# Kernel optimization log

Hardware: AMD Instinct MI355X
Metric: run time of the kernel (lower is better)

Reference implementation:

```python
import jax, jax.numpy as jnp
import numpy as np


def setup_inputs() -> dict:
    key = jax.random.key(0)
    k1, k2, k3 = jax.random.split(key, 3)
    B, H, L, OUT = 4096, 2048, 8, 1024
    x = jax.random.normal(k1, (B, H), dtype=jnp.float32)
    W = jax.random.normal(k2, (L, H, H), dtype=jnp.float32)
    beta = jax.random.normal(k3, (H, OUT), dtype=jnp.float32)
    return {"x": x, "W": W, "beta": beta}


def _fcn_forward(x, W, beta):
    h = W.shape[-1]
    scale = 1.0 / jnp.sqrt(jnp.asarray(h, x.dtype))
    # Linear1d: (x[:,None]*W).sum(-1)/sqrt(h) == x @ W.T / sqrt(h); then ReLU.
    def layer(y, Wi):
        y = jax.nn.relu(jnp.einsum('bi,oi->bo', y, Wi) * scale)
        return y, None
    y, _ = jax.lax.scan(layer, x, W)
    # readout: y @ beta / h
    return jnp.einsum('bh,ho->bo', y, beta) / h


def reference(x, W, beta):
    return _fcn_forward(x, W, beta)
```

## Files before the change

kernel.cpp:

```cpp
#include <hip/hip_runtime.h>
#include <cstdint>
#include <cstddef>

typedef __bf16          bf16x8  __attribute__((ext_vector_type(8)));
typedef float           f32x4   __attribute__((ext_vector_type(4)));
typedef unsigned short  u16x8   __attribute__((ext_vector_type(8)));

__device__ __forceinline__ unsigned short f32_bf16_rne(float f) {
  union { float f; unsigned u; } v; v.f = f;
  unsigned u = v.u + 0x7FFFu + ((v.u >> 16) & 1u);
  return (unsigned short)(u >> 16);
}

__global__ void cvt_f32_bf16(const float* __restrict__ in,
                             unsigned short* __restrict__ out, int n8) {
  int idx = blockIdx.x * 256 + threadIdx.x;
  int stride = gridDim.x * 256;
  for (int i = idx; i < n8; i += stride) {
    float4 a = ((const float4*)in)[2 * (size_t)i];
    float4 b = ((const float4*)in)[2 * (size_t)i + 1];
    u16x8 o;
    o[0] = f32_bf16_rne(a.x); o[1] = f32_bf16_rne(a.y);
    o[2] = f32_bf16_rne(a.z); o[3] = f32_bf16_rne(a.w);
    o[4] = f32_bf16_rne(b.x); o[5] = f32_bf16_rne(b.y);
    o[6] = f32_bf16_rne(b.z); o[7] = f32_bf16_rne(b.w);
    *(u16x8*)(out + (size_t)i * 8) = o;
  }
}

__global__ void cvt_transpose(const float* __restrict__ in,
                              unsigned short* __restrict__ out, int H, int O) {
  __shared__ float tile[32][33];
  int o0 = blockIdx.x * 32, h0 = blockIdx.y * 32;
  int tx = threadIdx.x & 31, ty = threadIdx.x >> 5;
  #pragma unroll
  for (int i = ty; i < 32; i += 8)
    tile[i][tx] = in[(size_t)(h0 + i) * O + (o0 + tx)];
  __syncthreads();
  #pragma unroll
  for (int i = ty; i < 32; i += 8)
    out[(size_t)(o0 + i) * H + (h0 + tx)] = f32_bf16_rne(tile[tx][i]);
}


#define GLOAD(gp, lp)                                                   \
  __builtin_amdgcn_global_load_lds(                                     \
      (const __attribute__((address_space(1))) void*)(gp),              \
      (__attribute__((address_space(3))) void*)(lp), 16, 0, 0)

#define MFMA16 __builtin_amdgcn_mfma_f32_16x16x32_bf16

#define PHASE(MH, STAGE)                                                      \
  do {                                                                        \
    bf16x8 a00 = *(const bf16x8*)(cA + aBase + ((MH)*2+0)*1024 + c0);         \
    bf16x8 a01 = *(const bf16x8*)(cA + aBase + ((MH)*2+0)*1024 + c1);         \
    bf16x8 a10 = *(const bf16x8*)(cA + aBase + ((MH)*2+1)*1024 + c0);         \
    bf16x8 a11 = *(const bf16x8*)(cA + aBase + ((MH)*2+1)*1024 + c1);         \
    bf16x8 b00 = *(const bf16x8*)(cB + bBase + 0*1024 + c0);                  \
    bf16x8 b01 = *(const bf16x8*)(cB + bBase + 0*1024 + c1);                  \
    bf16x8 b10 = *(const bf16x8*)(cB + bBase + 1*1024 + c0);                  \
    bf16x8 b11 = *(const bf16x8*)(cB + bBase + 1*1024 + c1);                  \
    bf16x8 b20 = *(const bf16x8*)(cB + bBase + 2*1024 + c0);                  \
    bf16x8 b21 = *(const bf16x8*)(cB + bBase + 2*1024 + c1);                  \
    bf16x8 b30 = *(const bf16x8*)(cB + bBase + 3*1024 + c0);                  \
    bf16x8 b31 = *(const bf16x8*)(cB + bBase + 3*1024 + c1);                  \
    STAGE                                                                     \
    __builtin_amdgcn_sched_barrier(0);                                        \
    __builtin_amdgcn_s_barrier();                                             \
    asm volatile("s_waitcnt lgkmcnt(0)" ::: "memory");                        \
    __builtin_amdgcn_sched_barrier(0);                                        \
    __builtin_amdgcn_s_setprio(1);                                            \
    acc[(MH)*2+0][0] = MFMA16(a00, b00, acc[(MH)*2+0][0], 0, 0, 0);           \
    acc[(MH)*2+0][1] = MFMA16(a00, b10, acc[(MH)*2+0][1], 0, 0, 0);           \
    acc[(MH)*2+0][2] = MFMA16(a00, b20, acc[(MH)*2+0][2], 0, 0, 0);           \
    acc[(MH)*2+0][3] = MFMA16(a00, b30, acc[(MH)*2+0][3], 0, 0, 0);           \
    acc[(MH)*2+1][0] = MFMA16(a10, b00, acc[(MH)*2+1][0], 0, 0, 0);           \
    acc[(MH)*2+1][1] = MFMA16(a10, b10, acc[(MH)*2+1][1], 0, 0, 0);           \
    acc[(MH)*2+1][2] = MFMA16(a10, b20, acc[(MH)*2+1][2], 0, 0, 0);           \
    acc[(MH)*2+1][3] = MFMA16(a10, b30, acc[(MH)*2+1][3], 0, 0, 0);           \
    acc[(MH)*2+0][0] = MFMA16(a01, b01, acc[(MH)*2+0][0], 0, 0, 0);           \
    acc[(MH)*2+0][1] = MFMA16(a01, b11, acc[(MH)*2+0][1], 0, 0, 0);           \
    acc[(MH)*2+0][2] = MFMA16(a01, b21, acc[(MH)*2+0][2], 0, 0, 0);           \
    acc[(MH)*2+0][3] = MFMA16(a01, b31, acc[(MH)*2+0][3], 0, 0, 0);           \
    acc[(MH)*2+1][0] = MFMA16(a11, b01, acc[(MH)*2+1][0], 0, 0, 0);           \
    acc[(MH)*2+1][1] = MFMA16(a11, b11, acc[(MH)*2+1][1], 0, 0, 0);           \
    acc[(MH)*2+1][2] = MFMA16(a11, b21, acc[(MH)*2+1][2], 0, 0, 0);           \
    acc[(MH)*2+1][3] = MFMA16(a11, b31, acc[(MH)*2+1][3], 0, 0, 0);           \
    __builtin_amdgcn_s_setprio(0);                                            \
    __builtin_amdgcn_sched_barrier(0);                                        \
    __builtin_amdgcn_s_barrier();                                             \
  } while (0)

__global__ __launch_bounds__(512, 2)
void gemm256x128(const unsigned short* __restrict__ A,
                 const unsigned short* __restrict__ B,
                 unsigned short* __restrict__ Cp, int N, int K, float scale) {
  __shared__ __bf16 As[3 * 256 * 64] __attribute__((aligned(16)));
  __shared__ __bf16 Bs[3 * 128 * 64] __attribute__((aligned(16)));

  const int tid  = threadIdx.x;
  const int lane = tid & 63;
  const int wave = tid >> 6;
  const int wr   = wave >> 1;
  const int wc   = wave & 1;
  const int l16  = lane & 15;
  const int kgrp = lane >> 4;

  const int p   = blockIdx.y * gridDim.x + blockIdx.x;
  const int lin = (p & 7) * (256 >> 3) + (p >> 3);
  const int brow0 = (lin >> 4) * 256;
  const int bcol0 = (lin & 15) * 128;

  const int xorv  = (l16 & 7) << 3;
  const int c0    = (kgrp * 8) ^ xorv;
  const int c1    = (32 + kgrp * 8) ^ xorv;
  const int aBase = (wr * 64 + l16) * 64;
  const int bBase = (wc * 64 + l16) * 64;

  const int srow = tid >> 3;
  const int scol = ((tid & 7) * 8) ^ ((srow & 7) << 3);
  const unsigned short* gA0 = A + (size_t)(brow0 +   0 + srow) * K + scol;
  const unsigned short* gA1 = A + (size_t)(brow0 +  64 + srow) * K + scol;
  const unsigned short* gA2 = A + (size_t)(brow0 + 128 + srow) * K + scol;
  const unsigned short* gA3 = A + (size_t)(brow0 + 192 + srow) * K + scol;
  const unsigned short* gB0 = B + (size_t)(bcol0 +   0 + srow) * K + scol;
  const unsigned short* gB1 = B + (size_t)(bcol0 +  64 + srow) * K + scol;

  f32x4 acc[4][4] = {};

  const int NT = K >> 6;

  {
    GLOAD(gA0, &As[0 * 4096 + tid * 8]);
    GLOAD(gA1, &As[1 * 4096 + tid * 8]);
    GLOAD(gA2, &As[2 * 4096 + tid * 8]);
    GLOAD(gA3, &As[3 * 4096 + tid * 8]);
    GLOAD(gB0, &Bs[0 * 4096 + tid * 8]);
    GLOAD(gB1, &Bs[1 * 4096 + tid * 8]);
    GLOAD(gA0 + 64, &As[16384 + 0 * 4096 + tid * 8]);
    GLOAD(gA1 + 64, &As[16384 + 1 * 4096 + tid * 8]);
    GLOAD(gA2 + 64, &As[16384 + 2 * 4096 + tid * 8]);
    GLOAD(gA3 + 64, &As[16384 + 3 * 4096 + tid * 8]);
    GLOAD(gB0 + 64, &Bs[8192 + 0 * 4096 + tid * 8]);
    GLOAD(gB1 + 64, &Bs[8192 + 1 * 4096 + tid * 8]);
    asm volatile("s_waitcnt vmcnt(6)" ::: "memory");
    __builtin_amdgcn_s_barrier();
  }

  int s = 0;
  for (int t = 0; t < NT; ++t) {
    const __bf16* cA = &As[s * 16384];
    const __bf16* cB = &Bs[s * 8192];
    int su = s + 2; if (su >= 3) su -= 3;
    __bf16* dA = &As[su * 16384];
    __bf16* dB = &Bs[su * 8192];
    const bool stg = (t < NT - 2);
    const size_t ko = (size_t)(t + 2) * 64;

    PHASE(0,
      if (stg) {
        GLOAD(gA0 + ko, dA + 0 * 4096 + tid * 8);
        GLOAD(gA1 + ko, dA + 1 * 4096 + tid * 8);
        GLOAD(gA2 + ko, dA + 2 * 4096 + tid * 8);
      }
    );
    PHASE(1,
      if (stg) {
        GLOAD(gA3 + ko, dA + 3 * 4096 + tid * 8);
        GLOAD(gB0 + ko, dB + 0 * 4096 + tid * 8);
        GLOAD(gB1 + ko, dB + 1 * 4096 + tid * 8);
        asm volatile("s_waitcnt vmcnt(6)" ::: "memory");
      } else if (t == NT - 2) {
        asm volatile("s_waitcnt vmcnt(0)" ::: "memory");
      }
    );
    s = s + 1; if (s == 3) s = 0;
  }

  const int crow0 = brow0 + wr * 64 + kgrp * 4;
  const int ccol0 = bcol0 + wc * 64 + l16;
  #pragma unroll
  for (int m = 0; m < 4; ++m)
    #pragma unroll
    for (int n = 0; n < 4; ++n)
      #pragma unroll
      for (int j = 0; j < 4; ++j) {
        float v = acc[m][n][j] * scale;
        v = v > 0.0f ? v : 0.0f;
        Cp[(size_t)(crow0 + m * 16 + j) * N + (ccol0 + n * 16)] = f32_bf16_rne(v);
      }
}

__global__ __launch_bounds__(256)
void gemm_bt_f32(const unsigned short* __restrict__ A,
                 const unsigned short* __restrict__ B,
                 float* __restrict__ C, int N, int K, float scale) {
  __shared__ __bf16 As[128 * 32] __attribute__((aligned(16)));
  __shared__ __bf16 Bs[128 * 32] __attribute__((aligned(16)));

  const int tid  = threadIdx.x;
  const int lane = tid & 63;
  const int wave = tid >> 6;
  const int wr   = wave >> 1, wc = wave & 1;
  const int l16  = lane & 15, kgrp = lane >> 4;

  const int brow0 = blockIdx.y * 128;
  const int bcol0 = blockIdx.x * 128;

  const int offb  = wave * 2048 + lane * 16;
  const int srow  = offb >> 6;
  const int selem = (offb & 63) >> 1;
  const unsigned short* gA0 = A + (size_t)(brow0 + srow) * K + selem;
  const unsigned short* gA1 = A + (size_t)(brow0 + srow + 16) * K + selem;
  const unsigned short* gB0 = B + (size_t)(bcol0 + srow) * K + selem;
  const unsigned short* gB1 = B + (size_t)(bcol0 + srow + 16) * K + selem;
  __bf16* lA0 = &As[wave * 1024];
  __bf16* lA1 = &As[wave * 1024 + 512];
  __bf16* lB0 = &Bs[wave * 1024];
  __bf16* lB1 = &Bs[wave * 1024 + 512];

  f32x4 acc[4][4] = {};
  const int aoff = (wr * 64 + l16) * 32 + kgrp * 8;
  const int boff = (wc * 64 + l16) * 32 + kgrp * 8;

  for (int k0 = 0; k0 < K; k0 += 32) {
    GLOAD(gA0 + k0, lA0);
    GLOAD(gA1 + k0, lA1);
    GLOAD(gB0 + k0, lB0);
    GLOAD(gB1 + k0, lB1);
    asm volatile("s_waitcnt vmcnt(0)" ::: "memory");
    __syncthreads();

    bf16x8 af[4], bfv[4];
    #pragma unroll
    for (int m = 0; m < 4; ++m)
      af[m] = *(const bf16x8*)(As + aoff + m * 16 * 32);
    #pragma unroll
    for (int n = 0; n < 4; ++n)
      bfv[n] = *(const bf16x8*)(Bs + boff + n * 16 * 32);
    #pragma unroll
    for (int m = 0; m < 4; ++m)
      #pragma unroll
      for (int n = 0; n < 4; ++n)
        acc[m][n] = MFMA16(af[m], bfv[n], acc[m][n], 0, 0, 0);
    __syncthreads();
  }

  const int crow0 = brow0 + wr * 64 + kgrp * 4;
  const int ccol0 = bcol0 + wc * 64 + l16;
  #pragma unroll
  for (int m = 0; m < 4; ++m)
    #pragma unroll
    for (int n = 0; n < 4; ++n)
      #pragma unroll
      for (int j = 0; j < 4; ++j)
        C[(size_t)(crow0 + m * 16 + j) * N + (ccol0 + n * 16)] =
            acc[m][n][j] * scale;
}

extern "C" void kernel_launch(void* const* d_in, const int* in_sizes, int n_in,
                              void* d_out, int out_size, void* d_ws, size_t ws_size,
                              hipStream_t stream) {
  const float* x    = (const float*)d_in[0];
  const float* W    = (const float*)d_in[1];
  const float* beta = (const float*)d_in[2];
  float* out = (float*)d_out;

  const int Bn = 4096, H = 2048, L = 8, O = 1024;

  unsigned short* y0    = (unsigned short*)d_ws;
  unsigned short* y1    = y0 + (size_t)Bn * H;
  unsigned short* Wb    = y1 + (size_t)Bn * H;
  unsigned short* betaT = Wb + (size_t)H * H;

  {
    int n8 = Bn * H / 8;
    int grid = (n8 + 255) / 256;
    if (grid > 2048) grid = 2048;
    cvt_f32_bf16<<<grid, 256, 0, stream>>>(x, y0, n8);
  }
  cvt_transpose<<<dim3(O / 32, H / 32), 256, 0, stream>>>(beta, betaT, H, O);

  const float s1 = 0.02209708691207961f;
  unsigned short* yin = y0;
  unsigned short* yout = y1;
  for (int l = 0; l < L; ++l) {
    int n8 = H * H / 8;
    int grid = (n8 + 255) / 256;
    if (grid > 2048) grid = 2048;
    cvt_f32_bf16<<<grid, 256, 0, stream>>>(W + (size_t)l * H * H, Wb, n8);
    gemm256x128<<<dim3(H / 128, Bn / 256), 512, 0, stream>>>(yin, Wb, yout, H, H, s1);
    unsigned short* t = yin; yin = yout; yout = t;
  }
  gemm_bt_f32<<<dim3(O / 128, Bn / 128), 256, 0, stream>>>(yin, betaT, out, O, H,
                                                           1.0f / 2048.0f);
}
```

Measured before the change: 428.9 us.

## Transpose GEMM block tile to 128x256 and split phases along K

```diff
diff --git a/kernel.cpp b/kernel.cpp
--- a/kernel.cpp
+++ b/kernel.cpp
@@ -42,7 +42,6 @@
     out[(size_t)(o0 + i) * H + (h0 + tx)] = f32_bf16_rne(tile[tx][i]);
 }
 
-
 #define GLOAD(gp, lp)                                                   \
   __builtin_amdgcn_global_load_lds(                                     \
       (const __attribute__((address_space(1))) void*)(gp),              \
@@ -50,70 +49,66 @@
 
 #define MFMA16 __builtin_amdgcn_mfma_f32_16x16x32_bf16
 
-#define PHASE(MH, STAGE)                                                      \
+
+#define PHASE(KK, STAGE)                                                      \
   do {                                                                        \
-    bf16x8 a00 = *(const bf16x8*)(cA + aBase + ((MH)*2+0)*1024 + c0);         \
-    bf16x8 a01 = *(const bf16x8*)(cA + aBase + ((MH)*2+0)*1024 + c1);         \
-    bf16x8 a10 = *(const bf16x8*)(cA + aBase + ((MH)*2+1)*1024 + c0);         \
-    bf16x8 a11 = *(const bf16x8*)(cA + aBase + ((MH)*2+1)*1024 + c1);         \
-    bf16x8 b00 = *(const bf16x8*)(cB + bBase + 0*1024 + c0);                  \
-    bf16x8 b01 = *(const bf16x8*)(cB + bBase + 0*1024 + c1);                  \
-    bf16x8 b10 = *(const bf16x8*)(cB + bBase + 1*1024 + c0);                  \
-    bf16x8 b11 = *(const bf16x8*)(cB + bBase + 1*1024 + c1);                  \
-    bf16x8 b20 = *(const bf16x8*)(cB + bBase + 2*1024 + c0);                  \
-    bf16x8 b21 = *(const bf16x8*)(cB + bBase + 2*1024 + c1);                  \
-    bf16x8 b30 = *(const bf16x8*)(cB + bBase + 3*1024 + c0);                  \
-    bf16x8 b31 = *(const bf16x8*)(cB + bBase + 3*1024 + c1);                  \
+    const int c = cc##KK;                                                     \
+    bf16x8 a0 = *(const bf16x8*)(cA + aBase + 0 * 1024 + c);                  \
+    bf16x8 a1 = *(const bf16x8*)(cA + aBase + 1 * 1024 + c);                  \
+    bf16x8 a2 = *(const bf16x8*)(cA + aBase + 2 * 1024 + c);                  \
+    bf16x8 a3 = *(const bf16x8*)(cA + aBase + 3 * 1024 + c);                  \
+    bf16x8 b0 = *(const bf16x8*)(cB + bBase + 0 * 1024 + c);                  \
+    bf16x8 b1 = *(const bf16x8*)(cB + bBase + 1 * 1024 + c);                  \
+    bf16x8 b2 = *(const bf16x8*)(cB + bBase + 2 * 1024 + c);                  \
+    bf16x8 b3 = *(const bf16x8*)(cB + bBase + 3 * 1024 + c);                  \
     STAGE                                                                     \
     __builtin_amdgcn_sched_barrier(0);                                        \
     __builtin_amdgcn_s_barrier();                                             \
     asm volatile("s_waitcnt lgkmcnt(0)" ::: "memory");                        \
     __builtin_amdgcn_sched_barrier(0);                                        \
     __builtin_amdgcn_s_setprio(1);                                            \
-    acc[(MH)*2+0][0] = MFMA16(a00, b00, acc[(MH)*2+0][0], 0, 0, 0);           \
-    acc[(MH)*2+0][1] = MFMA16(a00, b10, acc[(MH)*2+0][1], 0, 0, 0);           \
-    acc[(MH)*2+0][2] = MFMA16(a00, b20, acc[(MH)*2+0][2], 0, 0, 0);           \
-    acc[(MH)*2+0][3] = MFMA16(a00, b30, acc[(MH)*2+0][3], 0, 0, 0);           \
-    acc[(MH)*2+1][0] = MFMA16(a10, b00, acc[(MH)*2+1][0], 0, 0, 0);           \
-    acc[(MH)*2+1][1] = MFMA16(a10, b10, acc[(MH)*2+1][1], 0, 0, 0);           \
-    acc[(MH)*2+1][2] = MFMA16(a10, b20, acc[(MH)*2+1][2], 0, 0, 0);           \
-    acc[(MH)*2+1][3] = MFMA16(a10, b30, acc[(MH)*2+1][3], 0, 0, 0);           \
-    acc[(MH)*2+0][0] = MFMA16(a01, b01, acc[(MH)*2+0][0], 0, 0, 0);           \
-    acc[(MH)*2+0][1] = MFMA16(a01, b11, acc[(MH)*2+0][1], 0, 0, 0);           \
-    acc[(MH)*2+0][2] = MFMA16(a01, b21, acc[(MH)*2+0][2], 0, 0, 0);           \
-    acc[(MH)*2+0][3] = MFMA16(a01, b31, acc[(MH)*2+0][3], 0, 0, 0);           \
-    acc[(MH)*2+1][0] = MFMA16(a11, b01, acc[(MH)*2+1][0], 0, 0, 0);           \
-    acc[(MH)*2+1][1] = MFMA16(a11, b11, acc[(MH)*2+1][1], 0, 0, 0);           \
-    acc[(MH)*2+1][2] = MFMA16(a11, b21, acc[(MH)*2+1][2], 0, 0, 0);           \
-    acc[(MH)*2+1][3] = MFMA16(a11, b31, acc[(MH)*2+1][3], 0, 0, 0);           \
+    acc[0][0] = MFMA16(a0, b0, acc[0][0], 0, 0, 0);                           \
+    acc[0][1] = MFMA16(a0, b1, acc[0][1], 0, 0, 0);                           \
+    acc[0][2] = MFMA16(a0, b2, acc[0][2], 0, 0, 0);                           \
+    acc[0][3] = MFMA16(a0, b3, acc[0][3], 0, 0, 0);                           \
+    acc[1][0] = MFMA16(a1, b0, acc[1][0], 0, 0, 0);                           \
+    acc[1][1] = MFMA16(a1, b1, acc[1][1], 0, 0, 0);                           \
+    acc[1][2] = MFMA16(a1, b2, acc[1][2], 0, 0, 0);                           \
+    acc[1][3] = MFMA16(a1, b3, acc[1][3], 0, 0, 0);                           \
+    acc[2][0] = MFMA16(a2, b0, acc[2][0], 0, 0, 0);                           \
+    acc[2][1] = MFMA16(a2, b1, acc[2][1], 0, 0, 0);                           \
+    acc[2][2] = MFMA16(a2, b2, acc[2][2], 0, 0, 0);                           \
+    acc[2][3] = MFMA16(a2, b3, acc[2][3], 0, 0, 0);                           \
+    acc[3][0] = MFMA16(a3, b0, acc[3][0], 0, 0, 0);                           \
+    acc[3][1] = MFMA16(a3, b1, acc[3][1], 0, 0, 0);                           \
+    acc[3][2] = MFMA16(a3, b2, acc[3][2], 0, 0, 0);                           \
+    acc[3][3] = MFMA16(a3, b3, acc[3][3], 0, 0, 0);                           \
     __builtin_amdgcn_s_setprio(0);                                            \
     __builtin_amdgcn_sched_barrier(0);                                        \
     __builtin_amdgcn_s_barrier();                                             \
   } while (0)
 
 __global__ __launch_bounds__(512, 2)
-void gemm256x128(const unsigned short* __restrict__ A,
+void gemm128x256(const unsigned short* __restrict__ A,
                  const unsigned short* __restrict__ B,
                  unsigned short* __restrict__ Cp, int N, int K, float scale) {
-  __shared__ __bf16 As[3 * 256 * 64] __attribute__((aligned(16)));
-  __shared__ __bf16 Bs[3 * 128 * 64] __attribute__((aligned(16)));
+  __shared__ __bf16 As[3 * 128 * 64] __attribute__((aligned(16)));
+  __shared__ __bf16 Bs[3 * 256 * 64] __attribute__((aligned(16)));
 
   const int tid  = threadIdx.x;
   const int lane = tid & 63;
   const int wave = tid >> 6;
-  const int wr   = wave >> 1;
-  const int wc   = wave & 1;
+  const int wr   = wave >> 2;
+  const int wc   = wave & 3;
   const int l16  = lane & 15;
   const int kgrp = lane >> 4;
 
-  const int p   = blockIdx.y * gridDim.x + blockIdx.x;
-  const int lin = (p & 7) * (256 >> 3) + (p >> 3);
-  const int brow0 = (lin >> 4) * 256;
-  const int bcol0 = (lin & 15) * 128;
+  const int brow0 = blockIdx.y * 128;
+  const int bcol0 = blockIdx.x * 256;
 
   const int xorv  = (l16 & 7) << 3;
-  const int c0    = (kgrp * 8) ^ xorv;
-  const int c1    = (32 + kgrp * 8) ^ xorv;
+  const int cc0   = (kgrp * 8) ^ xorv;
+  const int cc1   = (32 + kgrp * 8) ^ xorv;
   const int aBase = (wr * 64 + l16) * 64;
   const int bBase = (wc * 64 + l16) * 64;
 
@@ -121,10 +116,10 @@
   const int scol = ((tid & 7) * 8) ^ ((srow & 7) << 3);
   const unsigned short* gA0 = A + (size_t)(brow0 +   0 + srow) * K + scol;
   const unsigned short* gA1 = A + (size_t)(brow0 +  64 + srow) * K + scol;
-  const unsigned short* gA2 = A + (size_t)(brow0 + 128 + srow) * K + scol;
-  const unsigned short* gA3 = A + (size_t)(brow0 + 192 + srow) * K + scol;
   const unsigned short* gB0 = B + (size_t)(bcol0 +   0 + srow) * K + scol;
   const unsigned short* gB1 = B + (size_t)(bcol0 +  64 + srow) * K + scol;
+  const unsigned short* gB2 = B + (size_t)(bcol0 + 128 + srow) * K + scol;
+  const unsigned short* gB3 = B + (size_t)(bcol0 + 192 + srow) * K + scol;
 
   f32x4 acc[4][4] = {};
 
@@ -133,27 +128,27 @@
   {
     GLOAD(gA0, &As[0 * 4096 + tid * 8]);
     GLOAD(gA1, &As[1 * 4096 + tid * 8]);
-    GLOAD(gA2, &As[2 * 4096 + tid * 8]);
-    GLOAD(gA3, &As[3 * 4096 + tid * 8]);
     GLOAD(gB0, &Bs[0 * 4096 + tid * 8]);
     GLOAD(gB1, &Bs[1 * 4096 + tid * 8]);
-    GLOAD(gA0 + 64, &As[16384 + 0 * 4096 + tid * 8]);
-    GLOAD(gA1 + 64, &As[16384 + 1 * 4096 + tid * 8]);
-    GLOAD(gA2 + 64, &As[16384 + 2 * 4096 + tid * 8]);
-    GLOAD(gA3 + 64, &As[16384 + 3 * 4096 + tid * 8]);
-    GLOAD(gB0 + 64, &Bs[8192 + 0 * 4096 + tid * 8]);
-    GLOAD(gB1 + 64, &Bs[8192 + 1 * 4096 + tid * 8]);
+    GLOAD(gB2, &Bs[2 * 4096 + tid * 8]);
+    GLOAD(gB3, &Bs[3 * 4096 + tid * 8]);
+    GLOAD(gA0 + 64, &As[8192 + 0 * 4096 + tid * 8]);
+    GLOAD(gA1 + 64, &As[8192 + 1 * 4096 + tid * 8]);
+    GLOAD(gB0 + 64, &Bs[16384 + 0 * 4096 + tid * 8]);
+    GLOAD(gB1 + 64, &Bs[16384 + 1 * 4096 + tid * 8]);
+    GLOAD(gB2 + 64, &Bs[16384 + 2 * 4096 + tid * 8]);
+    GLOAD(gB3 + 64, &Bs[16384 + 3 * 4096 + tid * 8]);
     asm volatile("s_waitcnt vmcnt(6)" ::: "memory");
     __builtin_amdgcn_s_barrier();
   }
 
   int s = 0;
   for (int t = 0; t < NT; ++t) {
-    const __bf16* cA = &As[s * 16384];
-    const __bf16* cB = &Bs[s * 8192];
+    const __bf16* cA = &As[s * 8192];
+    const __bf16* cB = &Bs[s * 16384];
     int su = s + 2; if (su >= 3) su -= 3;
-    __bf16* dA = &As[su * 16384];
-    __bf16* dB = &Bs[su * 8192];
+    __bf16* dA = &As[su * 8192];
+    __bf16* dB = &Bs[su * 16384];
     const bool stg = (t < NT - 2);
     const size_t ko = (size_t)(t + 2) * 64;
 
@@ -161,14 +156,14 @@
       if (stg) {
         GLOAD(gA0 + ko, dA + 0 * 4096 + tid * 8);
         GLOAD(gA1 + ko, dA + 1 * 4096 + tid * 8);
-        GLOAD(gA2 + ko, dA + 2 * 4096 + tid * 8);
+        GLOAD(gB0 + ko, dB + 0 * 4096 + tid * 8);
       }
     );
     PHASE(1,
       if (stg) {
-        GLOAD(gA3 + ko, dA + 3 * 4096 + tid * 8);
-        GLOAD(gB0 + ko, dB + 0 * 4096 + tid * 8);
         GLOAD(gB1 + ko, dB + 1 * 4096 + tid * 8);
+        GLOAD(gB2 + ko, dB + 2 * 4096 + tid * 8);
+        GLOAD(gB3 + ko, dB + 3 * 4096 + tid * 8);
         asm volatile("s_waitcnt vmcnt(6)" ::: "memory");
       } else if (t == NT - 2) {
         asm volatile("s_waitcnt vmcnt(0)" ::: "memory");
@@ -289,7 +284,7 @@
     int grid = (n8 + 255) / 256;
     if (grid > 2048) grid = 2048;
     cvt_f32_bf16<<<grid, 256, 0, stream>>>(W + (size_t)l * H * H, Wb, n8);
-    gemm256x128<<<dim3(H / 128, Bn / 256), 512, 0, stream>>>(yin, Wb, yout, H, H, s1);
+    gemm128x256<<<dim3(H / 256, Bn / 128), 512, 0, stream>>>(yin, Wb, yout, H, H, s1);
     unsigned short* t = yin; yin = yout; yout = t;
   }
   gemm_bt_f32<<<dim3(O / 128, Bn / 128), 256, 0, stream>>>(yin, betaT, out, O, H,
```

After: 408.5 us. 4.8% less time.
